# Kernel tuning notes

Measured on AMD Instinct MI355X. Metric: run time of the kernel, lower is better.

Reference implementation:

```python
import jax, jax.numpy as jnp
import numpy as np

N = 200000
E = 6400000


def setup_inputs() -> dict:
    key = jax.random.key(0)
    k1, k2, k3, k4 = jax.random.split(key, 4)
    x = jax.random.normal(k1, (N, 10), dtype=jnp.float32)
    edge_index = jax.random.randint(k2, (2, E), 0, N, dtype=jnp.int64)
    W1 = jax.random.normal(k3, (10, 16), dtype=jnp.float32) * (1.0 / np.sqrt(10))
    b1 = jnp.zeros((16,), dtype=jnp.float32)
    W2 = jax.random.normal(k4, (16, 2), dtype=jnp.float32) * (1.0 / np.sqrt(16))
    b2 = jnp.zeros((2,), dtype=jnp.float32)
    return {"x": x, "edge_index": edge_index, "W1": W1, "b1": b1, "W2": W2, "b2": b2}


def gcn_layer(x, src, dst, W, b, num_nodes):
    # GCNConv: out = D^{-1/2} (A + I) D^{-1/2} (x W) + b, deg computed on A+I
    loop = jnp.arange(num_nodes, dtype=src.dtype)
    s = jnp.concatenate([src, loop])
    d = jnp.concatenate([dst, loop])
    deg = jax.ops.segment_sum(jnp.ones(s.shape[0], dtype=x.dtype), d, num_segments=num_nodes)
    dinv = jnp.where(deg > 0, jax.lax.rsqrt(deg), 0.0)
    norm = dinv[s] * dinv[d]                      # [E+N]
    h = x @ W                                     # [N, out] (transform before gather)
    msg = h[s] * norm[:, None]                    # [E+N, out]
    return jax.ops.segment_sum(msg, d, num_segments=num_nodes) + b


def reference(x, edge_index, W1, b1, W2, b2):
    src, dst = edge_index[0], edge_index[1]
    n = x.shape[0]
    h = jax.nn.relu(gcn_layer(x, src, dst, W1, b1, n))
    return gcn_layer(h, src, dst, W2, b2, n)
```

## Files before the change

kernel.cpp:

```cpp
#include <hip/hip_runtime.h>
#include <hip/hip_fp16.h>

#define BLK 256
#define BBLK 512
#define ABLK 512
#define DBLK 512
#define NBK 782
#define BW 256
#define CAP 9984
#define NCH 3
#define CHUNK 6144


__global__ void k_hist(const int* __restrict__ dst, int e, int* __restrict__ gcnt,
                       int* __restrict__ blockhist) {
  __shared__ int h[NBK];
  for (int i = threadIdx.x; i < NBK; i += BLK) h[i] = 0;
  __syncthreads();
  int base = blockIdx.x * CHUNK;
  int m = min(CHUNK, e - base);
  for (int k = threadIdx.x; k < m; k += BLK) atomicAdd(&h[dst[base + k] >> 8], 1);
  __syncthreads();
  int* row = blockhist + (size_t)blockIdx.x * NBK;
  for (int b = threadIdx.x; b < NBK; b += BLK) {
    int c = h[b];
    row[b] = c;
    if (c) atomicAdd(&gcnt[b], c);
  }
}

__global__ void k_scan(const int* __restrict__ gcnt, int* __restrict__ gbase,
                       int* __restrict__ gcur, int e) {
  __shared__ int s[1024];
  int t = threadIdx.x;
  int v = (t < NBK) ? gcnt[t] : 0;
  s[t] = v;
  __syncthreads();
  for (int d = 1; d < 1024; d <<= 1) {
    int u = (t >= d) ? s[t - d] : 0;
    __syncthreads();
    s[t] += u;
    __syncthreads();
  }
  if (t < NBK) { int ex = s[t] - v; gbase[t] = ex; gcur[t] = ex; }
  if (t == 0) gbase[NBK] = e;
}

__global__ void __launch_bounds__(BBLK) k_bin(const int* __restrict__ src,
                                              const int* __restrict__ dst, int e,
                                              int* __restrict__ gcur,
                                              const int* __restrict__ blockhist,
                                              unsigned* __restrict__ binned) {
  __shared__ int lcnt[NBK];
  __shared__ int loff[NBK + 1];
  __shared__ int lbase[NBK];
  __shared__ int part[BBLK];
  __shared__ unsigned sorted[CHUNK];
  __shared__ unsigned short bkt16[CHUNK];
  int t = threadIdx.x;
  int base = blockIdx.x * CHUNK;
  int m = min(CHUNK, e - base);

  const int* row = blockhist + (size_t)blockIdx.x * NBK;
  for (int i = t; i < NBK; i += BBLK) lcnt[i] = row[i];
  __syncthreads();
  int b0 = 2 * t;
  int s0 = (b0 + 0 < NBK) ? lcnt[b0 + 0] : 0;
  int s1 = (b0 + 1 < NBK) ? lcnt[b0 + 1] : 0;
  int tsum = s0 + s1;
  part[t] = tsum;
  __syncthreads();
  for (int d = 1; d < BBLK; d <<= 1) {
    int u = (t >= d) ? part[t - d] : 0;
    __syncthreads();
    part[t] += u;
    __syncthreads();
  }
  int ex = part[t] - tsum;
  if (b0 + 0 < NBK) loff[b0 + 0] = ex;
  if (b0 + 1 < NBK) loff[b0 + 1] = ex + s0;
  if (t == 0) loff[NBK] = m;
  __syncthreads();
  for (int b = t; b < NBK; b += BBLK) {
    int c = lcnt[b];
    lbase[b] = c ? atomicAdd(&gcur[b], c) : 0;
  }
  __syncthreads();
  for (int b = t; b < NBK; b += BBLK) lcnt[b] = loff[b];
  __syncthreads();
  for (int k = t; k < m; k += BBLK) {
    int d = dst[base + k];
    int b = d >> 8;
    int dl = d & 255;
    int pos = atomicAdd(&lcnt[b], 1);
    sorted[pos] = (unsigned)src[base + k] | ((unsigned)dl << 18);
    bkt16[pos] = (unsigned short)b;
  }
  __syncthreads();
  for (int i = t; i < m; i += BBLK) {
    int b = bkt16[i];
    binned[lbase[b] + (i - loff[b])] = sorted[i];
  }
}

__global__ void __launch_bounds__(DBLK) k_ldeg_t1(const unsigned* __restrict__ binned,
                                                  const int* __restrict__ gbase,
                                                  const float* __restrict__ x,
                                                  const float* __restrict__ W1,
                                                  float* __restrict__ dinv,
                                                  __half* __restrict__ hs1, int n) {
  __shared__ int cnt[2][BW];
  __shared__ float w[160];
  int t = threadIdx.x;
  cnt[t >> 8][t & 255] = 0;
  if (t < 160) w[t] = W1[t];
  __syncthreads();
  int b = blockIdx.x;
  int p0 = gbase[b], p1 = gbase[b + 1];
  int h = t >> 8;
  for (int p = p0 + t; p < p1; p += DBLK) atomicAdd(&cnt[h][binned[p] >> 18], 1);
  __syncthreads();
  if (t >= BW) return;
  int v = b * BW + t;
  if (v >= n) return;
  float di = rsqrtf((float)(cnt[0][t] + cnt[1][t]) + 1.0f);
  dinv[v] = di;
  float xi[10];
#pragma unroll
  for (int k = 0; k < 10; k++) xi[k] = x[(size_t)v * 10 + k];
  __half2 hv[8];
#pragma unroll
  for (int j = 0; j < 8; j++) {
    float acc0 = 0.f, acc1 = 0.f;
#pragma unroll
    for (int k = 0; k < 10; k++) {
      acc0 = fmaf(xi[k], w[k * 16 + 2 * j], acc0);
      acc1 = fmaf(xi[k], w[k * 16 + 2 * j + 1], acc1);
    }
    hv[j] = __floats2half2_rn(acc0 * di, acc1 * di);
  }
  float4* o = (float4*)(hs1 + (size_t)v * 16);
  o[0] = *(float4*)&hv[0];
  o[1] = *(float4*)&hv[4];
}

__global__ void __launch_bounds__(ABLK) k_agg1s(unsigned* __restrict__ binned,
                                                const int* __restrict__ gbase,
                                                int* __restrict__ doff,
                                                const __half* __restrict__ hs1,
                                                const float* __restrict__ dinv,
                                                const float* __restrict__ b1,
                                                const float* __restrict__ W2,
                                                float* __restrict__ hs2, int n) {
  __shared__ int cnt[BW];
  __shared__ int stmp[BW];
  __shared__ int off[BW + 1];
  __shared__ int cur[BW];
  __shared__ int sorted[CAP];
  __shared__ float w2[32];
  __shared__ float sb1[16];
  int t = threadIdx.x;
  if (t < 32) w2[t] = W2[t];
  if (t >= 32 && t < 48) sb1[t - 32] = b1[t - 32];
  int bkt = blockIdx.x;
  int p0 = gbase[bkt], p1 = gbase[bkt + 1];
  const int j = t >> 1;
  const int c = t & 1;
  float acc[8];
#pragma unroll
  for (int q = 0; q < 8; q++) acc[q] = 0.f;

#define ACCR(R) { const __half2* h2_ = (const __half2*)&R; \
    float2 f0_ = __half22float2(h2_[0]); \
    float2 f1_ = __half22float2(h2_[1]); \
    float2 f2_ = __half22float2(h2_[2]); \
    float2 f3_ = __half22float2(h2_[3]); \
    acc[0] += f0_.x; acc[1] += f0_.y; acc[2] += f1_.x; acc[3] += f1_.y; \
    acc[4] += f2_.x; acc[5] += f2_.y; acc[6] += f3_.x; acc[7] += f3_.y; }

  int p = p0;
  int cidx = 0;
  while (p < p1) {
    int m = min(CAP, p1 - p);
    if (t < BW) cnt[t] = 0;
    __syncthreads();
    for (int i = t; i < m; i += ABLK) atomicAdd(&cnt[binned[p + i] >> 18], 1);
    __syncthreads();
    if (t < BW) stmp[t] = cnt[t];
    __syncthreads();
    for (int d = 1; d < BW; d <<= 1) {
      int u = 0;
      if (t < BW && t >= d) u = stmp[t - d];
      __syncthreads();
      if (t < BW) stmp[t] += u;
      __syncthreads();
    }
    if (t < BW) { int ex = stmp[t] - cnt[t]; off[t] = ex; cur[t] = ex; }
    if (t == 0) off[BW] = m;
    __syncthreads();
    for (int i = t; i < m; i += ABLK) {
      unsigned pk = binned[p + i];
      int pos = atomicAdd(&cur[pk >> 18], 1);
      sorted[pos] = (int)(pk & 0x3FFFF);
    }
    __syncthreads();
    for (int i = t; i < m; i += ABLK) binned[p + i] = (unsigned)sorted[i];
    if (cidx < NCH && t <= BW) doff[((size_t)bkt * NCH + cidx) * (BW + 1) + t] = off[t];
    int i0 = off[j], i1 = off[j + 1];
    int i = i0;
    for (; i + 3 < i1; i += 4) {
      int s0 = sorted[i + 0];
      int s1 = sorted[i + 1];
      int s2 = sorted[i + 2];
      int s3 = sorted[i + 3];
      float4 r0 = *(const float4*)(hs1 + (size_t)s0 * 16 + c * 8);
      float4 r1 = *(const float4*)(hs1 + (size_t)s1 * 16 + c * 8);
      float4 r2 = *(const float4*)(hs1 + (size_t)s2 * 16 + c * 8);
      float4 r3 = *(const float4*)(hs1 + (size_t)s3 * 16 + c * 8);
      ACCR(r0); ACCR(r1); ACCR(r2); ACCR(r3);
    }
    for (; i < i1; i++) {
      int s = sorted[i];
      float4 r = *(const float4*)(hs1 + (size_t)s * 16 + c * 8);
      ACCR(r);
    }
    __syncthreads();
    p += m;
    cidx++;
  }
#undef ACCR

  int v = bkt * BW + j;
  if (v < n) {
    float di = dinv[v];
    float4 sf = *(const float4*)(hs1 + (size_t)v * 16 + c * 8);
    const __half2* sh = (const __half2*)&sf;
    float h0c = 0.f, h1c = 0.f;
#pragma unroll
    for (int q = 0; q < 4; q++) {
      float2 sv = __half22float2(sh[q]);
      int f0 = c * 8 + 2 * q;
      int f1 = f0 + 1;
      float a0 = fmaxf(fmaf(di, acc[2 * q + 0] + sv.x, sb1[f0]), 0.f);
      float a1 = fmaxf(fmaf(di, acc[2 * q + 1] + sv.y, sb1[f1]), 0.f);
      h0c = fmaf(a0, w2[f0 * 2 + 0], fmaf(a1, w2[f1 * 2 + 0], h0c));
      h1c = fmaf(a0, w2[f0 * 2 + 1], fmaf(a1, w2[f1 * 2 + 1], h1c));
    }
    float h0 = h0c + __shfl_xor(h0c, 1);
    float h1 = h1c + __shfl_xor(h1c, 1);
    if (c == 0) {
      hs2[(size_t)v * 2 + 0] = h0 * di;
      hs2[(size_t)v * 2 + 1] = h1 * di;
    }
  }
}

__global__ void __launch_bounds__(BLK) k_agg2(const unsigned* __restrict__ binned,
                                              const int* __restrict__ gbase,
                                              const int* __restrict__ doff,
                                              const float* __restrict__ hs2,
                                              const float* __restrict__ dinv,
                                              const float* __restrict__ b2,
                                              float* __restrict__ out, int n) {
  int t = threadIdx.x;
  int bkt = blockIdx.x;
  int p0 = gbase[bkt], p1 = gbase[bkt + 1];
  float a0 = 0.f, a1 = 0.f;
  int cidx = 0;
  for (int p = p0; p < p1; p += CAP, cidx++) {
    const int* row = doff + ((size_t)bkt * NCH + cidx) * (BW + 1);
    int i0 = row[t], i1 = row[t + 1];
    const unsigned* bp = binned + p;
    int i = i0;
    for (; i + 3 < i1; i += 4) {
      int s0 = bp[i + 0];
      int s1 = bp[i + 1];
      int s2 = bp[i + 2];
      int s3 = bp[i + 3];
      float2 m0 = *(const float2*)(hs2 + (size_t)s0 * 2);
      float2 m1 = *(const float2*)(hs2 + (size_t)s1 * 2);
      float2 m2 = *(const float2*)(hs2 + (size_t)s2 * 2);
      float2 m3 = *(const float2*)(hs2 + (size_t)s3 * 2);
      a0 += m0.x + m1.x + m2.x + m3.x;
      a1 += m0.y + m1.y + m2.y + m3.y;
    }
    for (; i < i1; i++) {
      float2 m = *(const float2*)(hs2 + (size_t)bp[i] * 2);
      a0 += m.x;
      a1 += m.y;
    }
  }
  int v = bkt * BW + t;
  if (v < n) {
    float di = dinv[v];
    out[(size_t)v * 2 + 0] = fmaf(di, a0 + hs2[(size_t)v * 2 + 0], b2[0]);
    out[(size_t)v * 2 + 1] = fmaf(di, a1 + hs2[(size_t)v * 2 + 1], b2[1]);
  }
}

extern "C" void kernel_launch(void* const* d_in, const int* in_sizes, int n_in,
                              void* d_out, int out_size, void* d_ws, size_t ws_size,
                              hipStream_t stream) {
  const float* x  = (const float*)d_in[0];
  const int*   ei = (const int*)d_in[1];
  const float* W1 = (const float*)d_in[2];
  const float* b1 = (const float*)d_in[3];
  const float* W2 = (const float*)d_in[4];
  const float* b2 = (const float*)d_in[5];
  float* out = (float*)d_out;

  const int n = in_sizes[0] / 10;
  const int e = in_sizes[1] / 2;
  const int* src = ei;
  const int* dst = ei + e;

  int gC = (e + CHUNK - 1) / CHUNK;

  char* ws = (char*)d_ws;
  int*      gcnt      = (int*)ws;      ws += (size_t)NBK * 4;
  int*      gbase     = (int*)ws;      ws += ((size_t)NBK + 1) * 4;
  int*      gcur      = (int*)ws;      ws += (size_t)NBK * 4;
  int*      doff      = (int*)ws;      ws += (size_t)NBK * NCH * (BW + 1) * 4;
  int*      blockhist = (int*)ws;      ws += (size_t)gC * NBK * 4;
  unsigned* binned    = (unsigned*)ws; ws += (size_t)e * 4;
  float*    dinv      = (float*)ws;    ws += (size_t)n * 4;
  __half*   hs1       = (__half*)ws;   ws += (size_t)n * 16 * 2;
  float*    hs2       = (float*)ws;    ws += (size_t)n * 2 * 4;

  hipMemsetAsync(gcnt, 0, (size_t)NBK * 4, stream);
  k_hist<<<gC, BLK, 0, stream>>>(dst, e, gcnt, blockhist);
  k_scan<<<1, 1024, 0, stream>>>(gcnt, gbase, gcur, e);
  k_bin<<<gC, BBLK, 0, stream>>>(src, dst, e, gcur, blockhist, binned);
  k_ldeg_t1<<<NBK, DBLK, 0, stream>>>(binned, gbase, x, W1, dinv, hs1, n);
  k_agg1s<<<NBK, ABLK, 0, stream>>>(binned, gbase, doff, hs1, dinv, b1, W2, hs2, n);
  k_agg2<<<NBK, BLK, 0, stream>>>(binned, gbase, doff, hs2, dinv, b2, out, n);
}
```

Measured before the change: 349.8 us.

## Compute per-node degree with global atomics in histogram pass; reuse it downstream

The histogram kernel now also counts each node's in-degree with a global atomic per edge. This lets the transform kernel read degrees directly instead of rescanning the binned edges, and lets the aggregation kernel skip its counting pass when a bucket fits in one chunk. The bucket-to-global atomics are staggered per block to reduce contention, CAP is lowered, and the second aggregation uses two threads per node with a shuffle reduction. The cost is 6.4M extra global atomics spread over 200k addresses, plus a larger memset.

```diff
diff --git a/kernel.cpp b/kernel.cpp
--- a/kernel.cpp
+++ b/kernel.cpp
@@ -4,25 +4,30 @@
 #define BLK 256
 #define BBLK 512
 #define ABLK 512
-#define DBLK 512
 #define NBK 782
 #define BW 256
-#define CAP 9984
+#define CAP 8960
 #define NCH 3
 #define CHUNK 6144
 
 
 __global__ void k_hist(const int* __restrict__ dst, int e, int* __restrict__ gcnt,
-                       int* __restrict__ blockhist) {
+                       int* __restrict__ blockhist, int* __restrict__ deg) {
   __shared__ int h[NBK];
   for (int i = threadIdx.x; i < NBK; i += BLK) h[i] = 0;
   __syncthreads();
   int base = blockIdx.x * CHUNK;
   int m = min(CHUNK, e - base);
-  for (int k = threadIdx.x; k < m; k += BLK) atomicAdd(&h[dst[base + k] >> 8], 1);
+  for (int k = threadIdx.x; k < m; k += BLK) {
+    int d = dst[base + k];
+    atomicAdd(&h[d >> 8], 1);
+    atomicAdd(&deg[d], 1);
+  }
   __syncthreads();
   int* row = blockhist + (size_t)blockIdx.x * NBK;
-  for (int b = threadIdx.x; b < NBK; b += BLK) {
+  int sft = (blockIdx.x * 193) % NBK;
+  for (int bb = threadIdx.x; bb < NBK; bb += BLK) {
+    int b = bb + sft; if (b >= NBK) b -= NBK;
     int c = h[b];
     row[b] = c;
     if (c) atomicAdd(&gcnt[b], c);
@@ -81,7 +86,9 @@
   if (b0 + 1 < NBK) loff[b0 + 1] = ex + s0;
   if (t == 0) loff[NBK] = m;
   __syncthreads();
-  for (int b = t; b < NBK; b += BBLK) {
+  int sft = (blockIdx.x * 193) % NBK;
+  for (int bb = t; bb < NBK; bb += BBLK) {
+    int b = bb + sft; if (b >= NBK) b -= NBK;
     int c = lcnt[b];
     lbase[b] = c ? atomicAdd(&gcur[b], c) : 0;
   }
@@ -103,27 +110,18 @@
   }
 }
 
-__global__ void __launch_bounds__(DBLK) k_ldeg_t1(const unsigned* __restrict__ binned,
-                                                  const int* __restrict__ gbase,
-                                                  const float* __restrict__ x,
-                                                  const float* __restrict__ W1,
-                                                  float* __restrict__ dinv,
-                                                  __half* __restrict__ hs1, int n) {
-  __shared__ int cnt[2][BW];
+__global__ void __launch_bounds__(BLK) k_t1(const int* __restrict__ deg,
+                                            const float* __restrict__ x,
+                                            const float* __restrict__ W1,
+                                            float* __restrict__ dinv,
+                                            __half* __restrict__ hs1, int n) {
   __shared__ float w[160];
   int t = threadIdx.x;
-  cnt[t >> 8][t & 255] = 0;
   if (t < 160) w[t] = W1[t];
   __syncthreads();
-  int b = blockIdx.x;
-  int p0 = gbase[b], p1 = gbase[b + 1];
-  int h = t >> 8;
-  for (int p = p0 + t; p < p1; p += DBLK) atomicAdd(&cnt[h][binned[p] >> 18], 1);
-  __syncthreads();
-  if (t >= BW) return;
-  int v = b * BW + t;
+  int v = blockIdx.x * BLK + t;
   if (v >= n) return;
-  float di = rsqrtf((float)(cnt[0][t] + cnt[1][t]) + 1.0f);
+  float di = rsqrtf((float)deg[v] + 1.0f);
   dinv[v] = di;
   float xi[10];
 #pragma unroll
@@ -146,6 +144,7 @@
 
 __global__ void __launch_bounds__(ABLK) k_agg1s(unsigned* __restrict__ binned,
                                                 const int* __restrict__ gbase,
+                                                const int* __restrict__ deg,
                                                 int* __restrict__ doff,
                                                 const __half* __restrict__ hs1,
                                                 const float* __restrict__ dinv,
@@ -164,6 +163,7 @@
   if (t >= 32 && t < 48) sb1[t - 32] = b1[t - 32];
   int bkt = blockIdx.x;
   int p0 = gbase[bkt], p1 = gbase[bkt + 1];
+  const bool fast = (p1 - p0) <= CAP;
   const int j = t >> 1;
   const int c = t & 1;
   float acc[8];
@@ -182,9 +182,13 @@
   int cidx = 0;
   while (p < p1) {
     int m = min(CAP, p1 - p);
-    if (t < BW) cnt[t] = 0;
-    __syncthreads();
-    for (int i = t; i < m; i += ABLK) atomicAdd(&cnt[binned[p + i] >> 18], 1);
+    if (fast) {
+      if (t < BW) cnt[t] = deg[(bkt << 8) + t];
+    } else {
+      if (t < BW) cnt[t] = 0;
+      __syncthreads();
+      for (int i = t; i < m; i += ABLK) atomicAdd(&cnt[binned[p + i] >> 18], 1);
+    }
     __syncthreads();
     if (t < BW) stmp[t] = cnt[t];
     __syncthreads();
@@ -255,28 +259,30 @@
   }
 }
 
-__global__ void __launch_bounds__(BLK) k_agg2(const unsigned* __restrict__ binned,
-                                              const int* __restrict__ gbase,
-                                              const int* __restrict__ doff,
-                                              const float* __restrict__ hs2,
-                                              const float* __restrict__ dinv,
-                                              const float* __restrict__ b2,
-                                              float* __restrict__ out, int n) {
-  int t = threadIdx.x;
+__global__ void __launch_bounds__(BBLK) k_agg2(const unsigned* __restrict__ binned,
+                                               const int* __restrict__ gbase,
+                                               const int* __restrict__ doff,
+                                               const float* __restrict__ hs2,
+                                               const float* __restrict__ dinv,
+                                               const float* __restrict__ b2,
+                                               float* __restrict__ out, int n) {
+  int t = threadIdx.x;
+  int j = t >> 1;
+  int c = t & 1;
   int bkt = blockIdx.x;
   int p0 = gbase[bkt], p1 = gbase[bkt + 1];
   float a0 = 0.f, a1 = 0.f;
   int cidx = 0;
   for (int p = p0; p < p1; p += CAP, cidx++) {
     const int* row = doff + ((size_t)bkt * NCH + cidx) * (BW + 1);
-    int i0 = row[t], i1 = row[t + 1];
+    int i0 = row[j], i1 = row[j + 1];
     const unsigned* bp = binned + p;
-    int i = i0;
-    for (; i + 3 < i1; i += 4) {
+    int i = i0 + c;
+    for (; i + 6 < i1; i += 8) {
       int s0 = bp[i + 0];
-      int s1 = bp[i + 1];
-      int s2 = bp[i + 2];
-      int s3 = bp[i + 3];
+      int s1 = bp[i + 2];
+      int s2 = bp[i + 4];
+      int s3 = bp[i + 6];
       float2 m0 = *(const float2*)(hs2 + (size_t)s0 * 2);
       float2 m1 = *(const float2*)(hs2 + (size_t)s1 * 2);
       float2 m2 = *(const float2*)(hs2 + (size_t)s2 * 2);
@@ -284,14 +290,16 @@
       a0 += m0.x + m1.x + m2.x + m3.x;
       a1 += m0.y + m1.y + m2.y + m3.y;
     }
-    for (; i < i1; i++) {
+    for (; i < i1; i += 2) {
       float2 m = *(const float2*)(hs2 + (size_t)bp[i] * 2);
       a0 += m.x;
       a1 += m.y;
     }
   }
-  int v = bkt * BW + t;
-  if (v < n) {
+  a0 += __shfl_xor(a0, 1);
+  a1 += __shfl_xor(a1, 1);
+  int v = bkt * BW + j;
+  if (c == 0 && v < n) {
     float di = dinv[v];
     out[(size_t)v * 2 + 0] = fmaf(di, a0 + hs2[(size_t)v * 2 + 0], b2[0]);
     out[(size_t)v * 2 + 1] = fmaf(di, a1 + hs2[(size_t)v * 2 + 1], b2[1]);
@@ -318,6 +326,7 @@
 
   char* ws = (char*)d_ws;
   int*      gcnt      = (int*)ws;      ws += (size_t)NBK * 4;
+  int*      deg       = (int*)ws;      ws += (size_t)NBK * BW * 4;
   int*      gbase     = (int*)ws;      ws += ((size_t)NBK + 1) * 4;
   int*      gcur      = (int*)ws;      ws += (size_t)NBK * 4;
   int*      doff      = (int*)ws;      ws += (size_t)NBK * NCH * (BW + 1) * 4;
@@ -327,11 +336,11 @@
   __half*   hs1       = (__half*)ws;   ws += (size_t)n * 16 * 2;
   float*    hs2       = (float*)ws;    ws += (size_t)n * 2 * 4;
 
-  hipMemsetAsync(gcnt, 0, (size_t)NBK * 4, stream);
-  k_hist<<<gC, BLK, 0, stream>>>(dst, e, gcnt, blockhist);
+  hipMemsetAsync(gcnt, 0, ((size_t)NBK + (size_t)NBK * BW) * 4, stream);
+  k_hist<<<gC, BLK, 0, stream>>>(dst, e, gcnt, blockhist, deg);
   k_scan<<<1, 1024, 0, stream>>>(gcnt, gbase, gcur, e);
   k_bin<<<gC, BBLK, 0, stream>>>(src, dst, e, gcur, blockhist, binned);
-  k_ldeg_t1<<<NBK, DBLK, 0, stream>>>(binned, gbase, x, W1, dinv, hs1, n);
-  k_agg1s<<<NBK, ABLK, 0, stream>>>(binned, gbase, doff, hs1, dinv, b1, W2, hs2, n);
-  k_agg2<<<NBK, BLK, 0, stream>>>(binned, gbase, doff, hs2, dinv, b2, out, n);
-}
+  k_t1<<<NBK, BLK, 0, stream>>>(deg, x, W1, dinv, hs1, n);
+  k_agg1s<<<NBK, ABLK, 0, stream>>>(binned, gbase, deg, doff, hs1, dinv, b1, W2, hs2, n);
+  k_agg2<<<NBK, BBLK, 0, stream>>>(binned, gbase, doff, hs2, dinv, b2, out, n);
+}
```

Result: slower. 561.0 us (+60.4%).
